# Performance work log

Measured on AMD Instinct MI355X. Metric: run time of the kernel, lower is better.

The kernel has to match this reference:

```python
import jax, jax.numpy as jnp
import numpy as np

SEQ = 4096
E = 2048

def setup_inputs() -> dict:
    key = jax.random.key(0)
    kx, kq, kk, kv = jax.random.split(key, 4)
    scale = 1.0 / np.sqrt(E)
    x = jax.random.normal(kx, (SEQ, E), dtype=jnp.float32)
    # nn.Linear weights: shape [out, in], applied as x @ W.T
    Wq = jax.random.uniform(kq, (E, E), dtype=jnp.float32, minval=-scale, maxval=scale)
    Wk = jax.random.uniform(kk, (E, E), dtype=jnp.float32, minval=-scale, maxval=scale)
    Wv = jax.random.uniform(kv, (E, E), dtype=jnp.float32, minval=-scale, maxval=scale)
    return {"x": x, "Wq": Wq, "Wk": Wk, "Wv": Wv}

def reference(x, Wq, Wk, Wv):
    # q/k/v projections: nn.Linear(bias=False) -> x @ W.T
    q = x @ Wq.T  # [S, E]
    k = x @ Wk.T  # [S, E]
    v = x @ Wv.T  # [S, E]
    s = q @ k.T  # [S, S]
    w = jax.nn.softmax(s / jnp.sqrt(jnp.float32(E)), axis=-1)
    return w @ v  # [S, E]
```

## Files before the change

kernel.cpp:

```cpp
#include <hip/hip_runtime.h>
#include <hip/hip_bf16.h>

#define S_DIM 4096
#define E_DIM 2048

typedef __attribute__((ext_vector_type(4))) float f32x4;
typedef __attribute__((ext_vector_type(8))) short bf16x8;

__device__ __forceinline__ unsigned short f2bf(float f) {
  unsigned u = __builtin_bit_cast(unsigned, f);
  u += 0x7FFFu + ((u >> 16) & 1u);
  return (unsigned short)(u >> 16);
}
__device__ __forceinline__ float bf2f(unsigned short h) {
  return __builtin_bit_cast(float, ((unsigned)h) << 16);
}

__global__ __launch_bounds__(256) void cast_kernel(const float* __restrict__ in,
                                                   unsigned short* __restrict__ out,
                                                   int n4) {
  int i = blockIdx.x * 256 + threadIdx.x;
  if (i >= n4) return;
  float4 v = reinterpret_cast<const float4*>(in)[i];
  ushort4 o;
  o.x = f2bf(v.x); o.y = f2bf(v.y); o.z = f2bf(v.z); o.w = f2bf(v.w);
  reinterpret_cast<ushort4*>(out)[i] = o;
}

__global__ __launch_bounds__(256) void cast3_kernel(const float* __restrict__ w0,
                                                    const float* __restrict__ w1,
                                                    const float* __restrict__ w2,
                                                    unsigned short* __restrict__ out,
                                                    int n4each) {
  int i = blockIdx.x * 256 + threadIdx.x;
  if (i >= 3 * n4each) return;
  const float* src = (i < n4each) ? w0 : (i < 2 * n4each ? w1 : w2);
  int j = (i < n4each) ? i : (i < 2 * n4each ? i - n4each : i - 2 * n4each);
  float4 v = reinterpret_cast<const float4*>(src)[j];
  ushort4 o;
  o.x = f2bf(v.x); o.y = f2bf(v.y); o.z = f2bf(v.z); o.w = f2bf(v.w);
  reinterpret_cast<ushort4*>(out)[i] = o;
}

__global__ __launch_bounds__(256) void add_kernel(const float* __restrict__ a,
                                                  const float* __restrict__ b,
                                                  float* __restrict__ o, int n4) {
  int i = blockIdx.x * 256 + threadIdx.x;
  if (i >= n4) return;
  float4 va = reinterpret_cast<const float4*>(a)[i];
  float4 vb = reinterpret_cast<const float4*>(b)[i];
  float4 vo = {va.x + vb.x, va.y + vb.y, va.z + vb.z, va.w + vb.w};
  reinterpret_cast<float4*>(o)[i] = vo;
}


__device__ __forceinline__ void stage_half(const unsigned short* __restrict__ g,
                                           int grow0, int ld, int kByte0,
                                           char* ldsHalfBase, int tid) {
#pragma unroll
  for (int p = 0; p < 2; ++p) {
    const int o = (p * 512 + tid) * 16;
    const int S = o >> 10;
    const int oi = o & 1023;
    const int osi = oi ^ (((oi >> 9) & 1) << 5);
    const int r  = (S >> 1) * 16 + (osi >> 6);
    const int cb = (S & 1) * 64 + (osi & 63);
    const char* ga = reinterpret_cast<const char*>(g) +
                     ((size_t)(grow0 + r) * ld) * 2 + kByte0 + cb;
    char* la = ldsHalfBase + (o & ~1023);
    __builtin_amdgcn_global_load_lds(
        (const __attribute__((address_space(1))) void*)ga,
        (__attribute__((address_space(3))) void*)la, 16, 0, 0);
  }
}

#define MFMA_HALF(AM, AF)                                                      \
  _Pragma("unroll") for (int ks = 0; ks < 2; ++ks)                             \
  _Pragma("unroll") for (int mm = 0; mm < 4; ++mm) {                           \
    acc[(AM) + mm][0] = __builtin_amdgcn_mfma_f32_16x16x32_bf16(               \
        AF[mm][ks], b0[0][ks], acc[(AM) + mm][0], 0, 0, 0);                    \
    acc[(AM) + mm][1] = __builtin_amdgcn_mfma_f32_16x16x32_bf16(               \
        AF[mm][ks], b0[1][ks], acc[(AM) + mm][1], 0, 0, 0);                    \
    acc[(AM) + mm][2] = __builtin_amdgcn_mfma_f32_16x16x32_bf16(               \
        AF[mm][ks], b1[0][ks], acc[(AM) + mm][2], 0, 0, 0);                    \
    acc[(AM) + mm][3] = __builtin_amdgcn_mfma_f32_16x16x32_bf16(               \
        AF[mm][ks], b1[1][ks], acc[(AM) + mm][3], 0, 0, 0);                    \
  }

#define READ_A0(dst, buf)                                                      \
  _Pragma("unroll") for (int mm = 0; mm < 4; ++mm)                             \
  _Pragma("unroll") for (int ks = 0; ks < 2; ++ks)                             \
    dst[mm][ks] = *reinterpret_cast<const bf16x8*>(                            \
        (buf) + aBase + (mm * 2 + ks) * 1024 + rsw);

#define READ_A1(dst, buf)                                                      \
  _Pragma("unroll") for (int mm = 0; mm < 4; ++mm)                             \
  _Pragma("unroll") for (int ks = 0; ks < 2; ++ks)                             \
    dst[mm][ks] = *reinterpret_cast<const bf16x8*>(                            \
        (buf) + aBase + ((4 + mm) * 2 + ks) * 1024 + rsw);

#define READ_B(dst, buf, nh)                                                   \
  _Pragma("unroll") for (int nn = 0; nn < 2; ++nn)                             \
  _Pragma("unroll") for (int ks = 0; ks < 2; ++ks)                             \
    dst[nn][ks] = *reinterpret_cast<const bf16x8*>(                            \
        (buf) + bSub[nh][nn] + ks * 1024 + rsw);

enum { EPI_QKV = 0, EPI_BF16 = 1, EPI_F32 = 2 };

template <int EPI>
__global__ __launch_bounds__(512, 2) void gemm8(
    const unsigned short* __restrict__ A, const unsigned short* __restrict__ B,
    int lda, int ldb, int K,
    float* __restrict__ Cf, unsigned short* __restrict__ Cb,
    unsigned short* __restrict__ Ct, int ldc, float scale,
    int kElemPerZ, long long zStrideC) {
  extern __shared__ char lds[];

  const int tid = threadIdx.x;
  const int rowA0 = blockIdx.y * 256;
  const int rowB0 = blockIdx.x * 256;
  const int k0B = blockIdx.z * kElemPerZ * 2;
  if (EPI == EPI_F32) Cf += (size_t)blockIdx.z * zStrideC;

  const int wave = tid >> 6;
  const int lane = tid & 63;
  const int wm = wave >> 2;
  const int wn = wave & 3;
  const int l15 = lane & 15;
  const int kg = lane >> 4;
  const int rsw = (l15 * 64 + kg * 16) ^ ((l15 & 8) << 2);

  int bSub[2][2];
#pragma unroll
  for (int nh = 0; nh < 2; ++nh)
#pragma unroll
    for (int nn = 0; nn < 2; ++nn) {
      const int row = wn * 64 + nh * 32 + nn * 16;
      bSub[nh][nn] = 32768 + (row >> 7) * 16384 + ((row & 127) >> 4) * 2048;
    }
  const int aBase = wm * 16384;

  f32x4 acc[8][4];
#pragma unroll
  for (int mi = 0; mi < 8; ++mi)
#pragma unroll
    for (int ni = 0; ni < 4; ++ni) acc[mi][ni] = (f32x4){0.f, 0.f, 0.f, 0.f};

  const int NT = K / 64;
  char* buf0 = lds;
  char* buf1 = lds + 65536;

  stage_half(B, rowB0,       ldb, k0B,       buf0 + 32768, tid);
  stage_half(B, rowB0 + 128, ldb, k0B,       buf0 + 49152, tid);
  stage_half(A, rowA0,       lda, k0B,       buf0 + 0,     tid);
  stage_half(A, rowA0 + 128, lda, k0B,       buf0 + 16384, tid);
  stage_half(B, rowB0,       ldb, k0B + 128, buf1 + 32768, tid);
  stage_half(B, rowB0 + 128, ldb, k0B + 128, buf1 + 49152, tid);
  stage_half(A, rowA0,       lda, k0B + 128, buf1 + 0,     tid);
  asm volatile("s_waitcnt vmcnt(6)" ::: "memory");
  __builtin_amdgcn_sched_barrier(0);
  __builtin_amdgcn_s_barrier();

  for (int t = 0; t < NT; ++t) {
    char* bufc = lds + (t & 1) * 65536;
    char* bufn = lds + ((t & 1) ^ 1) * 65536;
    bf16x8 a0[4][2], a1[4][2], b0[2][2], b1[2][2];

    READ_A0(a0, bufc)
    READ_B(b0, bufc, 0)
    READ_B(b1, bufc, 1)
    if (t + 1 < NT)
      stage_half(A, rowA0 + 128, lda, k0B + (t + 1) * 128, bufn + 16384, tid);
    __builtin_amdgcn_sched_barrier(0);
    __builtin_amdgcn_s_barrier();
    asm volatile("s_waitcnt lgkmcnt(0)" ::: "memory");
    __builtin_amdgcn_sched_barrier(0);
    __builtin_amdgcn_s_setprio(1);
    MFMA_HALF(0, a0)
    __builtin_amdgcn_s_setprio(0);
    __builtin_amdgcn_s_barrier();

    READ_A1(a1, bufc)
    if (t + 2 < NT) {
      const int kb = k0B + (t + 2) * 128;
      stage_half(B, rowB0,       ldb, kb, bufc + 32768, tid);
      stage_half(B, rowB0 + 128, ldb, kb, bufc + 49152, tid);
      stage_half(A, rowA0,       lda, kb, bufc + 0,     tid);
      asm volatile("s_waitcnt vmcnt(6)" ::: "memory");
    } else {
      asm volatile("s_waitcnt vmcnt(0)" ::: "memory");
    }
    __builtin_amdgcn_sched_barrier(0);
    __builtin_amdgcn_s_barrier();
    asm volatile("s_waitcnt lgkmcnt(0)" ::: "memory");
    __builtin_amdgcn_sched_barrier(0);
    __builtin_amdgcn_s_setprio(1);
    MFMA_HALF(4, a1)
    __builtin_amdgcn_s_setprio(0);
    __builtin_amdgcn_s_barrier();
  }

  const int r0 = rowA0 + wm * 128;
  const int c0 = rowB0 + wn * 64;
#pragma unroll
  for (int mi = 0; mi < 8; ++mi) {
    const int row = r0 + (mi >> 2) * 64 + (mi & 3) * 16 + kg * 4;
#pragma unroll
    for (int ni = 0; ni < 4; ++ni) {
      const int col = c0 + (ni >> 1) * 32 + (ni & 1) * 16 + l15;
      f32x4 v = acc[mi][ni];
      if constexpr (EPI == EPI_F32) {
#pragma unroll
        for (int r = 0; r < 4; ++r)
          Cf[(size_t)(row + r) * ldc + col] = v[r];
      } else if constexpr (EPI == EPI_BF16) {
#pragma unroll
        for (int r = 0; r < 4; ++r)
          Cb[(size_t)(row + r) * ldc + col] = f2bf(v[r] * scale);
      } else {
        if (rowB0 < 4096) {
#pragma unroll
          for (int r = 0; r < 4; ++r)
            Cb[(size_t)(row + r) * 4096 + col] = f2bf(v[r]);
        } else {
          ushort4 pk;
          pk.x = f2bf(v[0]); pk.y = f2bf(v[1]);
          pk.z = f2bf(v[2]); pk.w = f2bf(v[3]);
          *reinterpret_cast<ushort4*>(Ct + (size_t)(col - 4096) * 4096 + row) = pk;
        }
      }
    }
  }
}

__global__ __launch_bounds__(256) void softmax_kernel(const unsigned short* __restrict__ Sm,
                                                      unsigned short* __restrict__ P) {
  const int row = blockIdx.x;
  const int tid = threadIdx.x;
  const unsigned short* src = Sm + (size_t)row * S_DIM;
  float vals[16];
  float mx = -1e30f;
#pragma unroll
  for (int i = 0; i < 4; ++i) {
    ushort4 h = reinterpret_cast<const ushort4*>(src)[tid + i * 256];
    float a = bf2f(h.x), b = bf2f(h.y), c = bf2f(h.z), d = bf2f(h.w);
    vals[i * 4 + 0] = a; vals[i * 4 + 1] = b;
    vals[i * 4 + 2] = c; vals[i * 4 + 3] = d;
    mx = fmaxf(mx, fmaxf(fmaxf(a, b), fmaxf(c, d)));
  }
#pragma unroll
  for (int off = 32; off >= 1; off >>= 1) mx = fmaxf(mx, __shfl_xor(mx, off, 64));
  __shared__ float red[8];
  const int wave = tid >> 6, lane = tid & 63;
  if (lane == 0) red[wave] = mx;
  __syncthreads();
  mx = fmaxf(fmaxf(red[0], red[1]), fmaxf(red[2], red[3]));
  float sum = 0.f;
#pragma unroll
  for (int i = 0; i < 16; ++i) { vals[i] = __expf(vals[i] - mx); sum += vals[i]; }
#pragma unroll
  for (int off = 32; off >= 1; off >>= 1) sum += __shfl_xor(sum, off, 64);
  if (lane == 0) red[4 + wave] = sum;
  __syncthreads();
  sum = red[4] + red[5] + red[6] + red[7];
  const float inv = 1.0f / sum;
  unsigned short* dst = P + (size_t)row * S_DIM;
#pragma unroll
  for (int i = 0; i < 4; ++i) {
    ushort4 pk;
    pk.x = f2bf(vals[i * 4 + 0] * inv);
    pk.y = f2bf(vals[i * 4 + 1] * inv);
    pk.z = f2bf(vals[i * 4 + 2] * inv);
    pk.w = f2bf(vals[i * 4 + 3] * inv);
    reinterpret_cast<ushort4*>(dst)[tid + i * 256] = pk;
  }
}

extern "C" void kernel_launch(void* const* d_in, const int* in_sizes, int n_in,
                              void* d_out, int out_size, void* d_ws, size_t ws_size,
                              hipStream_t stream) {
  const float* x  = (const float*)d_in[0];
  const float* Wq = (const float*)d_in[1];
  const float* Wk = (const float*)d_in[2];
  const float* Wv = (const float*)d_in[3];
  float* out = (float*)d_out;
  char* ws = (char*)d_ws;

  const size_t MB = 1024 * 1024;
  const size_t NEED = 120 * MB;
  if (ws_size < NEED) return;

  unsigned short* xb   = (unsigned short*)(ws);
  unsigned short* wcat = (unsigned short*)(ws + 16 * MB);
  unsigned short* qkb  = (unsigned short*)(ws + 40 * MB);
  unsigned short* vt   = (unsigned short*)(ws + 72 * MB);
  unsigned short* Sb   = (unsigned short*)(ws + 88 * MB);
  float* outp0 = (float*)(ws);
  float* outp1 = (float*)(ws + 88 * MB);
  unsigned short* P = qkb;

  hipFuncSetAttribute(reinterpret_cast<const void*>(&gemm8<EPI_QKV>),
                      hipFuncAttributeMaxDynamicSharedMemorySize, 131072);
  hipFuncSetAttribute(reinterpret_cast<const void*>(&gemm8<EPI_BF16>),
                      hipFuncAttributeMaxDynamicSharedMemorySize, 131072);
  hipFuncSetAttribute(reinterpret_cast<const void*>(&gemm8<EPI_F32>),
                      hipFuncAttributeMaxDynamicSharedMemorySize, 131072);

  const int nx4 = S_DIM * E_DIM / 4;
  const int nw4 = E_DIM * E_DIM / 4;

  cast_kernel<<<nx4 / 256, 256, 0, stream>>>(x, xb, nx4);
  cast3_kernel<<<3 * nw4 / 256, 256, 0, stream>>>(Wq, Wk, Wv, wcat, nw4);

  gemm8<EPI_QKV><<<dim3(24, 16, 1), 512, 131072, stream>>>(
      xb, wcat, E_DIM, E_DIM, E_DIM, nullptr, qkb, vt, 4096, 1.0f, 0, 0);

  const float scale = 0.022097086912079608f;
  gemm8<EPI_BF16><<<dim3(16, 16, 1), 512, 131072, stream>>>(
      qkb, qkb + 2048, 4096, 4096, E_DIM, nullptr, Sb, nullptr, 4096, scale, 0, 0);

  softmax_kernel<<<S_DIM, 256, 0, stream>>>(Sb, P);

  gemm8<EPI_F32><<<dim3(8, 16, 2), 512, 131072, stream>>>(
      P, vt, 4096, 4096, 2048, outp0, nullptr, nullptr, E_DIM, 1.0f,
      2048, (long long)(88 * MB) / 4);

  add_kernel<<<nx4 / 256, 256, 0, stream>>>(outp0, outp1, out, nx4);
}
```

Baseline: 398.1 us.

## Replace split-K PV GEMM and add kernel with a 256x128-tile full-K kernel

```diff
diff --git a/kernel.cpp b/kernel.cpp
--- a/kernel.cpp
+++ b/kernel.cpp
@@ -42,18 +42,6 @@
   reinterpret_cast<ushort4*>(out)[i] = o;
 }
 
-__global__ __launch_bounds__(256) void add_kernel(const float* __restrict__ a,
-                                                  const float* __restrict__ b,
-                                                  float* __restrict__ o, int n4) {
-  int i = blockIdx.x * 256 + threadIdx.x;
-  if (i >= n4) return;
-  float4 va = reinterpret_cast<const float4*>(a)[i];
-  float4 vb = reinterpret_cast<const float4*>(b)[i];
-  float4 vo = {va.x + vb.x, va.y + vb.y, va.z + vb.z, va.w + vb.w};
-  reinterpret_cast<float4*>(o)[i] = vo;
-}
-
-
 __device__ __forceinline__ void stage_half(const unsigned short* __restrict__ g,
                                            int grow0, int ld, int kByte0,
                                            char* ldsHalfBase, int tid) {
@@ -74,6 +62,7 @@
   }
 }
 
+
 #define MFMA_HALF(AM, AF)                                                      \
   _Pragma("unroll") for (int ks = 0; ks < 2; ++ks)                             \
   _Pragma("unroll") for (int mm = 0; mm < 4; ++mm) {                           \
@@ -105,22 +94,19 @@
     dst[nn][ks] = *reinterpret_cast<const bf16x8*>(                            \
         (buf) + bSub[nh][nn] + ks * 1024 + rsw);
 
-enum { EPI_QKV = 0, EPI_BF16 = 1, EPI_F32 = 2 };
+enum { EPI_QKV = 0, EPI_BF16 = 1 };
 
 template <int EPI>
 __global__ __launch_bounds__(512, 2) void gemm8(
     const unsigned short* __restrict__ A, const unsigned short* __restrict__ B,
     int lda, int ldb, int K,
-    float* __restrict__ Cf, unsigned short* __restrict__ Cb,
-    unsigned short* __restrict__ Ct, int ldc, float scale,
-    int kElemPerZ, long long zStrideC) {
+    unsigned short* __restrict__ Cb, unsigned short* __restrict__ Ct,
+    int ldc, float scale) {
   extern __shared__ char lds[];
 
   const int tid = threadIdx.x;
-  const int rowA0 = blockIdx.y * 256;
-  const int rowB0 = blockIdx.x * 256;
-  const int k0B = blockIdx.z * kElemPerZ * 2;
-  if (EPI == EPI_F32) Cf += (size_t)blockIdx.z * zStrideC;
+  const int rowA0 = blockIdx.x * 256;
+  const int rowB0 = blockIdx.y * 256;
 
   const int wave = tid >> 6;
   const int lane = tid & 63;
@@ -150,13 +136,13 @@
   char* buf0 = lds;
   char* buf1 = lds + 65536;
 
-  stage_half(B, rowB0,       ldb, k0B,       buf0 + 32768, tid);
-  stage_half(B, rowB0 + 128, ldb, k0B,       buf0 + 49152, tid);
-  stage_half(A, rowA0,       lda, k0B,       buf0 + 0,     tid);
-  stage_half(A, rowA0 + 128, lda, k0B,       buf0 + 16384, tid);
-  stage_half(B, rowB0,       ldb, k0B + 128, buf1 + 32768, tid);
-  stage_half(B, rowB0 + 128, ldb, k0B + 128, buf1 + 49152, tid);
-  stage_half(A, rowA0,       lda, k0B + 128, buf1 + 0,     tid);
+  stage_half(B, rowB0,       ldb, 0,   buf0 + 32768, tid);
+  stage_half(B, rowB0 + 128, ldb, 0,   buf0 + 49152, tid);
+  stage_half(A, rowA0,       lda, 0,   buf0 + 0,     tid);
+  stage_half(A, rowA0 + 128, lda, 0,   buf0 + 16384, tid);
+  stage_half(B, rowB0,       ldb, 128, buf1 + 32768, tid);
+  stage_half(B, rowB0 + 128, ldb, 128, buf1 + 49152, tid);
+  stage_half(A, rowA0,       lda, 128, buf1 + 0,     tid);
   asm volatile("s_waitcnt vmcnt(6)" ::: "memory");
   __builtin_amdgcn_sched_barrier(0);
   __builtin_amdgcn_s_barrier();
@@ -170,7 +156,7 @@
     READ_B(b0, bufc, 0)
     READ_B(b1, bufc, 1)
     if (t + 1 < NT)
-      stage_half(A, rowA0 + 128, lda, k0B + (t + 1) * 128, bufn + 16384, tid);
+      stage_half(A, rowA0 + 128, lda, (t + 1) * 128, bufn + 16384, tid);
     __builtin_amdgcn_sched_barrier(0);
     __builtin_amdgcn_s_barrier();
     asm volatile("s_waitcnt lgkmcnt(0)" ::: "memory");
@@ -182,7 +168,7 @@
 
     READ_A1(a1, bufc)
     if (t + 2 < NT) {
-      const int kb = k0B + (t + 2) * 128;
+      const int kb = (t + 2) * 128;
       stage_half(B, rowB0,       ldb, kb, bufc + 32768, tid);
       stage_half(B, rowB0 + 128, ldb, kb, bufc + 49152, tid);
       stage_half(A, rowA0,       lda, kb, bufc + 0,     tid);
@@ -209,11 +195,7 @@
     for (int ni = 0; ni < 4; ++ni) {
       const int col = c0 + (ni >> 1) * 32 + (ni & 1) * 16 + l15;
       f32x4 v = acc[mi][ni];
-      if constexpr (EPI == EPI_F32) {
-#pragma unroll
-        for (int r = 0; r < 4; ++r)
-          Cf[(size_t)(row + r) * ldc + col] = v[r];
-      } else if constexpr (EPI == EPI_BF16) {
+      if constexpr (EPI == EPI_BF16) {
 #pragma unroll
         for (int r = 0; r < 4; ++r)
           Cb[(size_t)(row + r) * ldc + col] = f2bf(v[r] * scale);
@@ -233,6 +215,122 @@
   }
 }
 
+__global__ __launch_bounds__(512, 2) void pv128(
+    const unsigned short* __restrict__ A, const unsigned short* __restrict__ B,
+    float* __restrict__ Cf) {
+  extern __shared__ char lds[];
+  const int tid = threadIdx.x;
+  const int rowA0 = blockIdx.x * 256;
+  const int colB0 = blockIdx.y * 128;
+  const int wave = tid >> 6, lane = tid & 63;
+  const int wm = wave >> 2, wn = wave & 3;
+  const int l15 = lane & 15, kg = lane >> 4;
+  const int rsw = (l15 * 64 + kg * 16) ^ ((l15 & 8) << 2);
+  const int aBase = wm * 16384;
+  const int bBase = 32768 + wn * 2 * 2048;
+
+  f32x4 acc[8][2];
+#pragma unroll
+  for (int mi = 0; mi < 8; ++mi) {
+    acc[mi][0] = (f32x4){0.f, 0.f, 0.f, 0.f};
+    acc[mi][1] = (f32x4){0.f, 0.f, 0.f, 0.f};
+  }
+
+  const int NT = S_DIM / 64;
+  char* buf0 = lds;
+  char* buf1 = lds + 49152;
+
+  stage_half(B, colB0,       S_DIM, 0,   buf0 + 32768, tid);
+  stage_half(A, rowA0,       S_DIM, 0,   buf0 + 0,     tid);
+  stage_half(A, rowA0 + 128, S_DIM, 0,   buf0 + 16384, tid);
+  stage_half(B, colB0,       S_DIM, 128, buf1 + 32768, tid);
+  stage_half(A, rowA0,       S_DIM, 128, buf1 + 0,     tid);
+  asm volatile("s_waitcnt vmcnt(4)" ::: "memory");
+  __builtin_amdgcn_sched_barrier(0);
+  __builtin_amdgcn_s_barrier();
+
+  for (int t = 0; t < NT; ++t) {
+    char* bufc = lds + (t & 1) * 49152;
+    char* bufn = lds + ((t & 1) ^ 1) * 49152;
+    bf16x8 a0[4][2], a1[4][2], bf[2][2];
+
+#pragma unroll
+    for (int mm = 0; mm < 4; ++mm)
+#pragma unroll
+      for (int ks = 0; ks < 2; ++ks)
+        a0[mm][ks] = *reinterpret_cast<const bf16x8*>(
+            bufc + aBase + mm * 2048 + ks * 1024 + rsw);
+#pragma unroll
+    for (int nn = 0; nn < 2; ++nn)
+#pragma unroll
+      for (int ks = 0; ks < 2; ++ks)
+        bf[nn][ks] = *reinterpret_cast<const bf16x8*>(
+            bufc + bBase + nn * 2048 + ks * 1024 + rsw);
+    if (t + 1 < NT)
+      stage_half(A, rowA0 + 128, S_DIM, (t + 1) * 128, bufn + 16384, tid);
+    __builtin_amdgcn_sched_barrier(0);
+    __builtin_amdgcn_s_barrier();
+    asm volatile("s_waitcnt lgkmcnt(0)" ::: "memory");
+    __builtin_amdgcn_sched_barrier(0);
+    __builtin_amdgcn_s_setprio(1);
+#pragma unroll
+    for (int ks = 0; ks < 2; ++ks)
+#pragma unroll
+      for (int mm = 0; mm < 4; ++mm) {
+        acc[mm][0] = __builtin_amdgcn_mfma_f32_16x16x32_bf16(
+            a0[mm][ks], bf[0][ks], acc[mm][0], 0, 0, 0);
+        acc[mm][1] = __builtin_amdgcn_mfma_f32_16x16x32_bf16(
+            a0[mm][ks], bf[1][ks], acc[mm][1], 0, 0, 0);
+      }
+    __builtin_amdgcn_s_setprio(0);
+    __builtin_amdgcn_s_barrier();
+
+#pragma unroll
+    for (int mm = 0; mm < 4; ++mm)
+#pragma unroll
+      for (int ks = 0; ks < 2; ++ks)
+        a1[mm][ks] = *reinterpret_cast<const bf16x8*>(
+            bufc + aBase + (4 + mm) * 2048 + ks * 1024 + rsw);
+    if (t + 2 < NT) {
+      const int kb = (t + 2) * 128;
+      stage_half(B, colB0, S_DIM, kb, bufc + 32768, tid);
+      stage_half(A, rowA0, S_DIM, kb, bufc + 0,     tid);
+      asm volatile("s_waitcnt vmcnt(4)" ::: "memory");
+    } else {
+      asm volatile("s_waitcnt vmcnt(0)" ::: "memory");
+    }
+    __builtin_amdgcn_sched_barrier(0);
+    __builtin_amdgcn_s_barrier();
+    asm volatile("s_waitcnt lgkmcnt(0)" ::: "memory");
+    __builtin_amdgcn_sched_barrier(0);
+    __builtin_amdgcn_s_setprio(1);
+#pragma unroll
+    for (int ks = 0; ks < 2; ++ks)
+#pragma unroll
+      for (int mm = 0; mm < 4; ++mm) {
+        acc[4 + mm][0] = __builtin_amdgcn_mfma_f32_16x16x32_bf16(
+            a1[mm][ks], bf[0][ks], acc[4 + mm][0], 0, 0, 0);
+        acc[4 + mm][1] = __builtin_amdgcn_mfma_f32_16x16x32_bf16(
+            a1[mm][ks], bf[1][ks], acc[4 + mm][1], 0, 0, 0);
+      }
+    __builtin_amdgcn_s_setprio(0);
+    __builtin_amdgcn_s_barrier();
+  }
+
+#pragma unroll
+  for (int mi = 0; mi < 8; ++mi) {
+    const int row = rowA0 + wm * 128 + mi * 16 + kg * 4;
+#pragma unroll
+    for (int ni = 0; ni < 2; ++ni) {
+      const int col = colB0 + wn * 32 + ni * 16 + l15;
+      f32x4 v = acc[mi][ni];
+#pragma unroll
+      for (int r = 0; r < 4; ++r)
+        Cf[(size_t)(row + r) * E_DIM + col] = v[r];
+    }
+  }
+}
+
 __global__ __launch_bounds__(256) void softmax_kernel(const unsigned short* __restrict__ Sm,
                                                       unsigned short* __restrict__ P) {
   const int row = blockIdx.x;
@@ -295,16 +393,14 @@
   unsigned short* qkb  = (unsigned short*)(ws + 40 * MB);
   unsigned short* vt   = (unsigned short*)(ws + 72 * MB);
   unsigned short* Sb   = (unsigned short*)(ws + 88 * MB);
-  float* outp0 = (float*)(ws);
-  float* outp1 = (float*)(ws + 88 * MB);
   unsigned short* P = qkb;
 
   hipFuncSetAttribute(reinterpret_cast<const void*>(&gemm8<EPI_QKV>),
                       hipFuncAttributeMaxDynamicSharedMemorySize, 131072);
   hipFuncSetAttribute(reinterpret_cast<const void*>(&gemm8<EPI_BF16>),
                       hipFuncAttributeMaxDynamicSharedMemorySize, 131072);
-  hipFuncSetAttribute(reinterpret_cast<const void*>(&gemm8<EPI_F32>),
-                      hipFuncAttributeMaxDynamicSharedMemorySize, 131072);
+  hipFuncSetAttribute(reinterpret_cast<const void*>(&pv128),
+                      hipFuncAttributeMaxDynamicSharedMemorySize, 98304);
 
   const int nx4 = S_DIM * E_DIM / 4;
   const int nw4 = E_DIM * E_DIM / 4;
@@ -312,18 +408,14 @@
   cast_kernel<<<nx4 / 256, 256, 0, stream>>>(x, xb, nx4);
   cast3_kernel<<<3 * nw4 / 256, 256, 0, stream>>>(Wq, Wk, Wv, wcat, nw4);
 
-  gemm8<EPI_QKV><<<dim3(24, 16, 1), 512, 131072, stream>>>(
-      xb, wcat, E_DIM, E_DIM, E_DIM, nullptr, qkb, vt, 4096, 1.0f, 0, 0);
+  gemm8<EPI_QKV><<<dim3(16, 24), 512, 131072, stream>>>(
+      xb, wcat, E_DIM, E_DIM, E_DIM, qkb, vt, 4096, 1.0f);
 
   const float scale = 0.022097086912079608f;
-  gemm8<EPI_BF16><<<dim3(16, 16, 1), 512, 131072, stream>>>(
-      qkb, qkb + 2048, 4096, 4096, E_DIM, nullptr, Sb, nullptr, 4096, scale, 0, 0);
+  gemm8<EPI_BF16><<<dim3(16, 16), 512, 131072, stream>>>(
+      qkb, qkb + 2048, 4096, 4096, E_DIM, Sb, nullptr, 4096, scale);
 
   softmax_kernel<<<S_DIM, 256, 0, stream>>>(Sb, P);
 
-  gemm8<EPI_F32><<<dim3(8, 16, 2), 512, 131072, stream>>>(
-      P, vt, 4096, 4096, 2048, outp0, nullptr, nullptr, E_DIM, 1.0f,
-      2048, (long long)(88 * MB) / 4);
-
-  add_kernel<<<nx4 / 256, 256, 0, stream>>>(outp0, outp1, out, nx4);
-}
+  pv128<<<dim3(16, 16), 512, 98304, stream>>>(P, vt, out);
+}
```

Measured after the change: 390.3 us. 1.02x faster.
